# Performance work log

Measured on AMD Instinct MI355X. Metric: run time of the kernel, lower is better.

Reference implementation:

```python
import jax, jax.numpy as jnp
import numpy as np


def setup_inputs() -> dict:
    key = jax.random.key(0)
    k1, k2, k3, k4 = jax.random.split(key, 4)
    B, C, H, W = 4, 256, 64, 64
    Va = jax.random.normal(k1, (B, C, H, W), jnp.float32)
    Vb = jax.random.normal(k2, (B, C, H, W), jnp.float32)
    # nn.Linear(C, C, bias=False) weight, used as x @ W^T
    W_linear = jax.random.normal(k3, (C, C), jnp.float32) * 0.05
    # nn.Conv2d(C, 1, 1, bias=False) weight, init normal_(0, 0.01)
    W_gate = jax.random.normal(k4, (C,), jnp.float32) * 0.01
    return {"Va_output": Va, "Vb_output": Vb, "W_linear": W_linear,
            "W_gate": W_gate, "input_size": 512}


def reference(Va_output, Vb_output, W_linear, W_gate, input_size):
    B, C, H, W = Vb_output.shape
    A = H * W  # all_dim
    Va_flat = Va_output.reshape(B, C, A)  # [B, C, A]
    Vb_flat = Vb_output.reshape(B, C, A)
    # linear on transposed A-major tokens: Va_t @ W_linear^T -> [B, A, C]
    Va_corr = jnp.einsum('bca,dc->bad', Va_flat, W_linear)
    # correlation matrix S = Va_corr @ Vb_flat -> [B, A, A]
    S = jnp.einsum('bac,can->ban'[:3] + 'c,c' if False else 'bac,cn', Va_corr, Vb_flat) if False else jnp.einsum('bac,bcn->ban', Va_corr, Vb_flat)
    # S_c = softmax(S, dim=1); S_r = softmax(S^T, dim=1) = softmax(S, axis=2)^T
    S_c = jax.nn.softmax(S, axis=1)
    S_r = jnp.swapaxes(jax.nn.softmax(S, axis=2), 1, 2)
    Vb_att = jnp.einsum('bca,ban->bcn', Va_flat, S_r).reshape(B, C, H, W)
    Va_att = jnp.einsum('bca,ban->bcn', Vb_flat, S_c).reshape(B, C, H, W)
    # 1x1 gate conv (C -> 1, no bias) + sigmoid
    Va_mask = jax.nn.sigmoid(jnp.einsum('bchw,c->bhw', Va_att, W_gate))[:, None]
    Vb_mask = jax.nn.sigmoid(jnp.einsum('bchw,c->bhw', Vb_att, W_gate))[:, None]
    Va_out = jnp.concatenate([Va_att * Va_mask, Va_output], axis=1)  # [B, 2C, H, W]
    Vb_out = jnp.concatenate([Vb_att * Vb_mask, Vb_output], axis=1)
    return (Va_out, Vb_out, input_size)
```

## Files before the change

kernel.cpp:

```cpp
#include <hip/hip_runtime.h>

typedef _Float16 f16;
typedef f16 f16x8 __attribute__((ext_vector_type(8)));
typedef float f32x4 __attribute__((ext_vector_type(4)));
typedef short b16x8 __attribute__((ext_vector_type(8)));
typedef unsigned short u16;
typedef u16 u16x4 __attribute__((ext_vector_type(4)));

#define MFMA_F16(a,b,c)  __builtin_amdgcn_mfma_f32_16x16x32_f16((a),(b),(c),0,0,0)
#define MFMA_BF16(a,b,c) __builtin_amdgcn_mfma_f32_16x16x32_bf16((a),(b),(c),0,0,0)

static __device__ __forceinline__ u16 bf16rn(float f) {
    unsigned u = __builtin_bit_cast(unsigned, f);
    u += 0x7FFFu + ((u >> 16) & 1u);
    return (u16)(u >> 16);
}

typedef const __attribute__((address_space(1))) unsigned int* gas_p;
typedef __attribute__((address_space(3))) unsigned int* las_p;
static __device__ __forceinline__ void gll16(const void* g, void* l) {
    __builtin_amdgcn_global_load_lds((gas_p)g, (las_p)l, 16, 0, 0);
}

static constexpr int B_ = 4, C_ = 256, A_ = 4096;
static constexpr int CA   = C_ * A_;
static constexpr int BCA  = B_ * CA;
static constexpr int OUT_T = B_ * 2 * CA;
static constexpr size_t WS_Va16 = 0;
static constexpr size_t WS_Vb16 = WS_Va16 + (size_t)BCA;
static constexpr size_t WS_VaT  = WS_Vb16 + (size_t)BCA;
static constexpr size_t WS_VbT  = WS_VaT  + (size_t)BCA;
static constexpr size_t WS_Q1   = WS_VbT  + (size_t)BCA;
static constexpr size_t WS_W16  = WS_Q1   + (size_t)BCA;
static constexpr size_t WS_HALFS = WS_W16 + (size_t)(C_ * C_);

static constexpr float M0 = 48.0f;

__global__ void coatt_convw(const float* __restrict__ W, f16* __restrict__ W16) {
    int i = blockIdx.x * 256 + threadIdx.x;
    W16[i] = (f16)W[i];
}

__global__ void coatt_transpose(const float* __restrict__ Va,
                                const float* __restrict__ Vb,
                                u16* __restrict__ ws) {
    __shared__ f16 tile[64][72];
    int z = blockIdx.z; int b = z >> 1; int which = z & 1;
    const float* src = which ? Vb : Va;
    u16* cm = ws + (which ? WS_Vb16 : WS_Va16);
    f16* am = (f16*)(ws + (which ? WS_VbT : WS_VaT));
    int a0 = blockIdx.x * 64, c0 = blockIdx.y * 64;
    int t = threadIdx.x;
    int r = t >> 2, q = t & 3;

    const float* sp = src + (size_t)(b * C_ + c0 + r) * A_ + a0 + q * 16;
    f16 h[16] __attribute__((aligned(16)));
    u16 hb[16] __attribute__((aligned(16)));
#pragma unroll
    for (int i = 0; i < 4; ++i) {
        float4 v = *(const float4*)(sp + i * 4);
        h[i*4+0] = (f16)v.x; h[i*4+1] = (f16)v.y;
        h[i*4+2] = (f16)v.z; h[i*4+3] = (f16)v.w;
        hb[i*4+0] = bf16rn(v.x); hb[i*4+1] = bf16rn(v.y);
        hb[i*4+2] = bf16rn(v.z); hb[i*4+3] = bf16rn(v.w);
    }
    u16* cp = cm + (size_t)(b * C_ + c0 + r) * A_ + a0 + q * 16;
    *(u16x4*)(cp)      = *(const u16x4*)&hb[0];
    *(u16x4*)(cp + 4)  = *(const u16x4*)&hb[4];
    *(u16x4*)(cp + 8)  = *(const u16x4*)&hb[8];
    *(u16x4*)(cp + 12) = *(const u16x4*)&hb[12];
#pragma unroll
    for (int i = 0; i < 16; ++i) tile[r][q * 16 + i] = h[i];
    __syncthreads();
    f16 ht[16] __attribute__((aligned(16)));
#pragma unroll
    for (int i = 0; i < 16; ++i) ht[i] = tile[q * 16 + i][r];
    f16* ap = am + (size_t)(b * A_ + a0 + r) * C_ + c0 + q * 16;
    *(f16x8*)(ap)     = *(const f16x8*)&ht[0];
    *(f16x8*)(ap + 8) = *(const f16x8*)&ht[8];
}

__global__ __launch_bounds__(256) void coatt_q1(const f16* __restrict__ vat,
                                                const f16* __restrict__ w16,
                                                f16* __restrict__ q1) {
    int b = blockIdx.y; int a0 = blockIdx.x * 64;
    int tid = threadIdx.x, wave = tid >> 6, lane = tid & 63;
    int m = lane & 15, quad = lane >> 4;

    const f16* Ap = vat + (size_t)(b * A_ + a0 + wave * 16 + m) * C_ + quad * 8;
    f16x8 af[8];
#pragma unroll
    for (int kc = 0; kc < 8; ++kc) af[kc] = *(const f16x8*)(Ap + kc * 32);

    f32x4 acc[16];
#pragma unroll
    for (int t = 0; t < 16; ++t) acc[t] = (f32x4){0.f, 0.f, 0.f, 0.f};

#pragma unroll
    for (int kc = 0; kc < 8; ++kc) {
#pragma unroll
        for (int t = 0; t < 16; ++t) {
            f16x8 bf = *(const f16x8*)(w16 + (size_t)(t * 16 + m) * C_ + kc * 32 + quad * 8);
            acc[t] = MFMA_F16(af[kc], bf, acc[t]);
        }
    }
#pragma unroll
    for (int t = 0; t < 16; ++t) {
#pragma unroll
        for (int r = 0; r < 4; ++r) {
            int arow = a0 + wave * 16 + quad * 4 + r;
            q1[(size_t)(b * A_ + arow) * C_ + t * 16 + m] = (f16)acc[t][r];
        }
    }
}

__global__ __launch_bounds__(512, 2) void coatt_flash(const u16* __restrict__ ws,
                                                      const float* __restrict__ Wgate,
                                                      float* __restrict__ dout) {
    __shared__ __align__(16) char smem[151552];
    char* Plds = smem + 131072;
    float* Lsum = (float*)(smem + 149504);
    float* Gsum = (float*)(smem + 150528);
    float* Olds = (float*)smem;

    int p = blockIdx.x;
    int vc = p & 7;
    int b = vc & 3, att = vc >> 2;
    int n0 = (p >> 3) * 128;

    const f16 *Qp, *Kp; const u16* Vp; float* outp;
    if (att == 0) {
        Qp = (const f16*)(ws + WS_Q1)  + (size_t)b * CA;
        Kp = (const f16*)(ws + WS_VbT) + (size_t)b * CA;
        Vp = ws + WS_Va16 + (size_t)b * CA;
        outp = dout + (size_t)OUT_T + (size_t)b * 2 * CA;
    } else {
        Qp = (const f16*)(ws + WS_VbT) + (size_t)b * CA;
        Kp = (const f16*)(ws + WS_Q1)  + (size_t)b * CA;
        Vp = ws + WS_Vb16 + (size_t)b * CA;
        outp = dout + (size_t)b * 2 * CA;
    }

    int tid = threadIdx.x, wave = tid >> 6, lane = tid & 63;
    int i = wave >> 1, j = wave & 1;
    int m = lane & 15, quad = lane >> 4;

    f16x8 qf[2][8];
#pragma unroll
    for (int qt = 0; qt < 2; ++qt) {
        const f16* qr = Qp + (size_t)(n0 + i * 32 + qt * 16 + m) * C_ + quad * 8;
#pragma unroll
        for (int kc = 0; kc < 8; ++kc) qf[qt][kc] = *(const f16x8*)(qr + kc * 32);
    }

    f32x4 Oacc[2][8];
#pragma unroll
    for (int qt = 0; qt < 2; ++qt)
#pragma unroll
        for (int ct = 0; ct < 8; ++ct) Oacc[qt][ct] = (f32x4){0.f, 0.f, 0.f, 0.f};
    float lpart[2] = {0.f, 0.f};

    int kch = (lane & 31) ^ ((2 * wave + (lane >> 5)) & 7);
    int vch = (lane & 7) ^ ((lane >> 3) & 7);
    const f16* kgb = Kp + (size_t)(2 * wave + (lane >> 5)) * C_ + kch * 8;
    const u16* vgb = Vp + (size_t)(8 * wave + (lane >> 3)) * A_ + vch * 8;

    {
        const f16* kg = kgb;
        char* kl = smem + wave * 1024;
#pragma unroll
        for (int ii = 0; ii < 4; ++ii) gll16(kg + ii * 16 * C_, kl + ii * 8192);
        const u16* vg = vgb;
        char* vl = smem + 65536 + wave * 1024;
#pragma unroll
        for (int ii = 0; ii < 4; ++ii) gll16(vg + (size_t)ii * 64 * A_, vl + ii * 8192);
    }

    for (int kb = 0; kb < 64; ++kb) {
        int cur = kb & 1, nxt = cur ^ 1;
        char* Kc = smem + cur * 32768;
        char* Vc = smem + 65536 + cur * 32768;
        __syncthreads();

        if (kb < 63) {
            const f16* kg = kgb + (size_t)(kb + 1) * 64 * C_;
            char* kl = smem + nxt * 32768 + wave * 1024;
#pragma unroll
            for (int ii = 0; ii < 4; ++ii) gll16(kg + ii * 16 * C_, kl + ii * 8192);
        }

        f32x4 Sc[2][2];
#pragma unroll
        for (int kt = 0; kt < 2; ++kt)
#pragma unroll
            for (int qt = 0; qt < 2; ++qt) Sc[kt][qt] = (f32x4){0.f, 0.f, 0.f, 0.f};
#pragma unroll
        for (int kc = 0; kc < 8; ++kc) {
            f16x8 kf[2];
#pragma unroll
            for (int kt = 0; kt < 2; ++kt) {
                int kl_ = j * 32 + kt * 16 + m;
                kf[kt] = *(const f16x8*)(Kc + kl_ * 512 +
                                         (((kc * 4 + quad) ^ (kl_ & 7)) << 4));
            }
#pragma unroll
            for (int kt = 0; kt < 2; ++kt)
#pragma unroll
                for (int qt = 0; qt < 2; ++qt)
                    Sc[kt][qt] = MFMA_F16(kf[kt], qf[qt][kc], Sc[kt][qt]);
        }

#pragma unroll
        for (int qt = 0; qt < 2; ++qt) {
            int qg = i * 32 + qt * 16 + m;
#pragma unroll
            for (int kt = 0; kt < 2; ++kt) {
                u16x4 pk;
                float s4 = 0.f;
#pragma unroll
                for (int r = 0; r < 4; ++r) {
                    float pv = __expf(Sc[kt][qt][r] - M0);
                    s4 += pv;
                    pk[r] = bf16rn(pv);
                }
                lpart[qt] += s4;
                *(u16x4*)(Plds + qg * 144 + (j * 32 + kt * 16 + quad * 4) * 2) = pk;
            }
        }
        __syncthreads();

        if (kb < 63) {
            const u16* vg = vgb + (size_t)(kb + 1) * 64;
            char* vl = smem + 65536 + nxt * 32768 + wave * 1024;
#pragma unroll
            for (int ii = 0; ii < 4; ++ii) gll16(vg + (size_t)ii * 64 * A_, vl + ii * 8192);
        }

#pragma unroll
        for (int kt = 0; kt < 2; ++kt) {
            b16x8 pf[2];
#pragma unroll
            for (int qt = 0; qt < 2; ++qt) {
                int qg = i * 32 + qt * 16 + m;
                pf[qt] = *(const b16x8*)(Plds + qg * 144 + kt * 64 + quad * 16);
            }
#pragma unroll
            for (int ct = 0; ct < 8; ++ct) {
                int c = j * 128 + ct * 16 + m;
                b16x8 vf = *(const b16x8*)(Vc + c * 128 +
                                           (((kt * 4 + quad) ^ (c & 7)) << 4));
#pragma unroll
                for (int qt = 0; qt < 2; ++qt)
                    Oacc[qt][ct] = MFMA_BF16(pf[qt], vf, Oacc[qt][ct]);
            }
        }
    }

#pragma unroll
    for (int qt = 0; qt < 2; ++qt) {
        float v = lpart[qt];
        v += __shfl_xor(v, 16);
        v += __shfl_xor(v, 32);
        lpart[qt] = v;
    }
    __syncthreads();
    if (lane < 16) {
#pragma unroll
        for (int qt = 0; qt < 2; ++qt)
            Lsum[j * 128 + i * 32 + qt * 16 + lane] = lpart[qt];
    }
    __syncthreads();
    float inv[2][4];
#pragma unroll
    for (int qt = 0; qt < 2; ++qt)
#pragma unroll
        for (int r = 0; r < 4; ++r) {
            int q = i * 32 + qt * 16 + quad * 4 + r;
            inv[qt][r] = 1.0f / (Lsum[q] + Lsum[128 + q]);
        }
    float gp[2][4] = {{0.f,0.f,0.f,0.f},{0.f,0.f,0.f,0.f}};
#pragma unroll
    for (int ct = 0; ct < 8; ++ct) {
        float w = Wgate[j * 128 + ct * 16 + m];
#pragma unroll
        for (int qt = 0; qt < 2; ++qt)
#pragma unroll
            for (int r = 0; r < 4; ++r) {
                float o = Oacc[qt][ct][r] * inv[qt][r];
                Oacc[qt][ct][r] = o;
                gp[qt][r] += o * w;
            }
    }
#pragma unroll
    for (int qt = 0; qt < 2; ++qt)
#pragma unroll
        for (int r = 0; r < 4; ++r) {
            float v = gp[qt][r];
            v += __shfl_xor(v, 1); v += __shfl_xor(v, 2);
            v += __shfl_xor(v, 4); v += __shfl_xor(v, 8);
            gp[qt][r] = v;
        }
    if (m == 0) {
#pragma unroll
        for (int qt = 0; qt < 2; ++qt)
#pragma unroll
            for (int r = 0; r < 4; ++r)
                Gsum[j * 128 + i * 32 + qt * 16 + quad * 4 + r] = gp[qt][r];
    }
    __syncthreads();
#pragma unroll
    for (int qt = 0; qt < 2; ++qt)
#pragma unroll
        for (int r = 0; r < 4; ++r) {
            int q = i * 32 + qt * 16 + quad * 4 + r;
            float g = Gsum[q] + Gsum[128 + q];
            float msk = 1.0f / (1.0f + __expf(-g));
#pragma unroll
            for (int ct = 0; ct < 8; ++ct) Oacc[qt][ct][r] *= msk;
        }

    for (int hf = 0; hf < 2; ++hf) {
        __syncthreads();
        if (j == hf) {
#pragma unroll
            for (int ct = 0; ct < 8; ++ct)
#pragma unroll
                for (int qt = 0; qt < 2; ++qt)
#pragma unroll
                    for (int r = 0; r < 4; ++r)
                        Olds[(ct * 16 + m) * 132 + i * 32 + qt * 16 + quad * 4 + r] =
                            Oacc[qt][ct][r];
        }
        __syncthreads();
#pragma unroll
        for (int ii = 0; ii < 8; ++ii) {
            int ci = tid + ii * 512;
            int c = ci >> 5, ch = (ci & 31) * 4;
            float4 v = *(const float4*)(Olds + c * 132 + ch);
            *(float4*)(outp + (size_t)(hf * 128 + c) * A_ + n0 + ch) = v;
        }
    }
}

__global__ void coatt_copy(const float* __restrict__ Va, const float* __restrict__ Vb,
                           const int* __restrict__ psz, float* __restrict__ dout) {
    int base = blockIdx.x * 256 + threadIdx.x;
    const float4* va4 = (const float4*)Va;
    const float4* vb4 = (const float4*)Vb;
    float4* out4 = (float4*)dout;
#pragma unroll
    for (int i = 0; i < 4; ++i) {
        int idx = base + i * 524288;
        int t = idx >> 20;
        int r = idx & 1048575;
        int b = r >> 18;
        int rr = r & 262143;
        float4 v = t ? vb4[r] : va4[r];
        out4[(size_t)t * 2097152 + (size_t)b * 524288 + 262144 + rr] = v;
    }
    if (base == 0) dout[16777216] = (float)(*psz);
}

extern "C" void kernel_launch(void* const* d_in, const int* in_sizes, int n_in,
                              void* d_out, int out_size, void* d_ws, size_t ws_size,
                              hipStream_t stream) {
    const float* Va = (const float*)d_in[0];
    const float* Vb = (const float*)d_in[1];
    const float* Wl = (const float*)d_in[2];
    const float* Wg = (const float*)d_in[3];
    const int* psz  = (const int*)d_in[4];
    float* out = (float*)d_out;
    u16* ws = (u16*)d_ws;

    if (ws_size < WS_HALFS * sizeof(u16)) return;

    coatt_convw<<<256, 256, 0, stream>>>(Wl, (f16*)(ws + WS_W16));
    coatt_transpose<<<dim3(64, 4, 8), 256, 0, stream>>>(Va, Vb, ws);
    coatt_q1<<<dim3(64, 4), 256, 0, stream>>>((const f16*)(ws + WS_VaT),
                                              (const f16*)(ws + WS_W16),
                                              (f16*)(ws + WS_Q1));
    coatt_flash<<<256, 512, 0, stream>>>(ws, Wg, out);
    coatt_copy<<<2048, 256, 0, stream>>>(Va, Vb, psz, out);
}
```

Baseline: 271.0 us.

## Pre-tile Q/K/V into MFMA-friendly blocked layout and retile flash waves 2x4

The transpose and Q1 kernels now write the K/Q and V operands in a blocked 64-row tile layout, 16-byte chunks grouped by channel-chunk, so the flash kernel can fill LDS with contiguous per-lane global_load_lds copies and read fragments without XOR swizzling. The flash kernel's wave grid changes from 4x2 to 2x4: each wave now covers 64 queries by 16 keys for S and 64 queries by 64 channels for O, so each K fragment is reused across four query tiles. Partial softmax sums and gate sums are now reduced across four waves, and outputs go to LDS as float4 stores. This is meant to cut LDS address arithmetic, bank conflicts and strided global loads, at the cost of more query-fragment registers per wave and a possibly different LDS bank-conflict pattern.

```diff
diff --git a/kernel.cpp b/kernel.cpp
--- a/kernel.cpp
+++ b/kernel.cpp
@@ -44,11 +44,11 @@
 __global__ void coatt_transpose(const float* __restrict__ Va,
                                 const float* __restrict__ Vb,
                                 u16* __restrict__ ws) {
-    __shared__ f16 tile[64][72];
+    __shared__ f16 tile[64][73];
     int z = blockIdx.z; int b = z >> 1; int which = z & 1;
     const float* src = which ? Vb : Va;
-    u16* cm = ws + (which ? WS_Vb16 : WS_Va16);
-    f16* am = (f16*)(ws + (which ? WS_VbT : WS_VaT));
+    char* vt = (char*)(ws + (which ? WS_Vb16 : WS_Va16)) + (size_t)b * CA * 2;
+    char* kt = (char*)(ws + (which ? WS_VbT : WS_VaT)) + (size_t)b * CA * 2;
     int a0 = blockIdx.x * 64, c0 = blockIdx.y * 64;
     int t = threadIdx.x;
     int r = t >> 2, q = t & 3;
@@ -64,33 +64,35 @@
         hb[i*4+0] = bf16rn(v.x); hb[i*4+1] = bf16rn(v.y);
         hb[i*4+2] = bf16rn(v.z); hb[i*4+3] = bf16rn(v.w);
     }
-    u16* cp = cm + (size_t)(b * C_ + c0 + r) * A_ + a0 + q * 16;
-    *(u16x4*)(cp)      = *(const u16x4*)&hb[0];
-    *(u16x4*)(cp + 4)  = *(const u16x4*)&hb[4];
-    *(u16x4*)(cp + 8)  = *(const u16x4*)&hb[8];
-    *(u16x4*)(cp + 12) = *(const u16x4*)&hb[12];
+    char* vb8 = vt + (size_t)(a0 >> 6) * 32768 + (c0 + r) * 16;
+    *(u16x4*)(vb8 + (q * 2 + 0) * 4096 + 0) = *(const u16x4*)&hb[0];
+    *(u16x4*)(vb8 + (q * 2 + 0) * 4096 + 8) = *(const u16x4*)&hb[4];
+    *(u16x4*)(vb8 + (q * 2 + 1) * 4096 + 0) = *(const u16x4*)&hb[8];
+    *(u16x4*)(vb8 + (q * 2 + 1) * 4096 + 8) = *(const u16x4*)&hb[12];
 #pragma unroll
     for (int i = 0; i < 16; ++i) tile[r][q * 16 + i] = h[i];
     __syncthreads();
     f16 ht[16] __attribute__((aligned(16)));
 #pragma unroll
     for (int i = 0; i < 16; ++i) ht[i] = tile[q * 16 + i][r];
-    f16* ap = am + (size_t)(b * A_ + a0 + r) * C_ + c0 + q * 16;
-    *(f16x8*)(ap)     = *(const f16x8*)&ht[0];
-    *(f16x8*)(ap + 8) = *(const f16x8*)&ht[8];
-}
-
-__global__ __launch_bounds__(256) void coatt_q1(const f16* __restrict__ vat,
-                                                const f16* __restrict__ w16,
-                                                f16* __restrict__ q1) {
+    char* kb8 = kt + (size_t)(a0 >> 6) * 32768 + r * 16;
+    *(f16x8*)(kb8 + (size_t)(c0 / 8 + q * 2 + 0) * 1024) = *(const f16x8*)&ht[0];
+    *(f16x8*)(kb8 + (size_t)(c0 / 8 + q * 2 + 1) * 1024) = *(const f16x8*)&ht[8];
+}
+
+__global__ __launch_bounds__(256) void coatt_q1(const u16* __restrict__ ws_) {
+    const char* vat = (const char*)(ws_ + WS_VaT);
+    const f16* w16 = (const f16*)(ws_ + WS_W16);
+    char* q1 = (char*)(ws_ + WS_Q1);
     int b = blockIdx.y; int a0 = blockIdx.x * 64;
     int tid = threadIdx.x, wave = tid >> 6, lane = tid & 63;
     int m = lane & 15, quad = lane >> 4;
 
-    const f16* Ap = vat + (size_t)(b * A_ + a0 + wave * 16 + m) * C_ + quad * 8;
+    const char* Ab = vat + (size_t)b * CA * 2 + (size_t)(a0 >> 6) * 32768;
     f16x8 af[8];
 #pragma unroll
-    for (int kc = 0; kc < 8; ++kc) af[kc] = *(const f16x8*)(Ap + kc * 32);
+    for (int kc = 0; kc < 8; ++kc)
+        af[kc] = *(const f16x8*)(Ab + (kc * 4 + quad) * 1024 + (wave * 16 + m) * 16);
 
     f32x4 acc[16];
 #pragma unroll
@@ -104,12 +106,16 @@
             acc[t] = MFMA_F16(af[kc], bf, acc[t]);
         }
     }
+    char* Qb = q1 + (size_t)b * CA * 2 + (size_t)(a0 >> 6) * 32768;
 #pragma unroll
     for (int t = 0; t < 16; ++t) {
 #pragma unroll
         for (int r = 0; r < 4; ++r) {
-            int arow = a0 + wave * 16 + quad * 4 + r;
-            q1[(size_t)(b * A_ + arow) * C_ + t * 16 + m] = (f16)acc[t][r];
+            int al = wave * 16 + quad * 4 + r;
+            int d = t * 16 + m;
+            f16 v = (f16)acc[t][r];
+            *(u16*)(Qb + (size_t)(d >> 3) * 1024 + al * 16 + (d & 7) * 2) =
+                __builtin_bit_cast(u16, v);
         }
     }
 }
@@ -117,10 +123,10 @@
 __global__ __launch_bounds__(512, 2) void coatt_flash(const u16* __restrict__ ws,
                                                       const float* __restrict__ Wgate,
                                                       float* __restrict__ dout) {
-    __shared__ __align__(16) char smem[151552];
+    __shared__ __align__(16) char smem[153600];
     char* Plds = smem + 131072;
     float* Lsum = (float*)(smem + 149504);
-    float* Gsum = (float*)(smem + 150528);
+    float* Gsum = (float*)(smem + 151552);
     float* Olds = (float*)smem;
 
     int p = blockIdx.x;
@@ -128,52 +134,53 @@
     int b = vc & 3, att = vc >> 2;
     int n0 = (p >> 3) * 128;
 
-    const f16 *Qp, *Kp; const u16* Vp; float* outp;
+    const char *Qp, *Kp, *Vp; float* outp;
+    const char* base = (const char*)ws;
+    size_t boff = (size_t)b * CA * 2;
     if (att == 0) {
-        Qp = (const f16*)(ws + WS_Q1)  + (size_t)b * CA;
-        Kp = (const f16*)(ws + WS_VbT) + (size_t)b * CA;
-        Vp = ws + WS_Va16 + (size_t)b * CA;
+        Qp = base + WS_Q1 * 2 + boff;
+        Kp = base + WS_VbT * 2 + boff;
+        Vp = base + WS_Va16 * 2 + boff;
         outp = dout + (size_t)OUT_T + (size_t)b * 2 * CA;
     } else {
-        Qp = (const f16*)(ws + WS_VbT) + (size_t)b * CA;
-        Kp = (const f16*)(ws + WS_Q1)  + (size_t)b * CA;
-        Vp = ws + WS_Vb16 + (size_t)b * CA;
+        Qp = base + WS_VbT * 2 + boff;
+        Kp = base + WS_Q1 * 2 + boff;
+        Vp = base + WS_Vb16 * 2 + boff;
         outp = dout + (size_t)b * 2 * CA;
     }
 
     int tid = threadIdx.x, wave = tid >> 6, lane = tid & 63;
-    int i = wave >> 1, j = wave & 1;
+    int iq = wave >> 2, jq = wave & 3;
     int m = lane & 15, quad = lane >> 4;
 
-    f16x8 qf[2][8];
-#pragma unroll
-    for (int qt = 0; qt < 2; ++qt) {
-        const f16* qr = Qp + (size_t)(n0 + i * 32 + qt * 16 + m) * C_ + quad * 8;
-#pragma unroll
-        for (int kc = 0; kc < 8; ++kc) qf[qt][kc] = *(const f16x8*)(qr + kc * 32);
-    }
-
-    f32x4 Oacc[2][8];
-#pragma unroll
-    for (int qt = 0; qt < 2; ++qt)
-#pragma unroll
-        for (int ct = 0; ct < 8; ++ct) Oacc[qt][ct] = (f32x4){0.f, 0.f, 0.f, 0.f};
-    float lpart[2] = {0.f, 0.f};
-
-    int kch = (lane & 31) ^ ((2 * wave + (lane >> 5)) & 7);
-    int vch = (lane & 7) ^ ((lane >> 3) & 7);
-    const f16* kgb = Kp + (size_t)(2 * wave + (lane >> 5)) * C_ + kch * 8;
-    const u16* vgb = Vp + (size_t)(8 * wave + (lane >> 3)) * A_ + vch * 8;
-
+    f16x8 qf[4][8];
     {
-        const f16* kg = kgb;
-        char* kl = smem + wave * 1024;
-#pragma unroll
-        for (int ii = 0; ii < 4; ++ii) gll16(kg + ii * 16 * C_, kl + ii * 8192);
-        const u16* vg = vgb;
-        char* vl = smem + 65536 + wave * 1024;
-#pragma unroll
-        for (int ii = 0; ii < 4; ++ii) gll16(vg + (size_t)ii * 64 * A_, vl + ii * 8192);
+        const char* qb = Qp + (size_t)((n0 >> 6) + iq) * 32768;
+#pragma unroll
+        for (int qt = 0; qt < 4; ++qt)
+#pragma unroll
+            for (int kc = 0; kc < 8; ++kc)
+                qf[qt][kc] = *(const f16x8*)(qb + (kc * 4 + quad) * 1024 +
+                                             (qt * 16 + m) * 16);
+    }
+
+    f32x4 Oacc[4][4];
+#pragma unroll
+    for (int qt = 0; qt < 4; ++qt)
+#pragma unroll
+        for (int ct = 0; ct < 4; ++ct) Oacc[qt][ct] = (f32x4){0.f, 0.f, 0.f, 0.f};
+    float lpart[4] = {0.f, 0.f, 0.f, 0.f};
+
+    const char* ksrc = Kp + wave * 1024 + lane * 16;
+    const char* vsrc = Vp + wave * 1024 + lane * 16;
+
+    {
+#pragma unroll
+        for (int ii = 0; ii < 4; ++ii)
+            gll16(ksrc + ii * 8192, smem + wave * 1024 + ii * 8192);
+#pragma unroll
+        for (int ii = 0; ii < 4; ++ii)
+            gll16(vsrc + ii * 8192, smem + 65536 + wave * 1024 + ii * 8192);
     }
 
     for (int kb = 0; kb < 64; ++kb) {
@@ -183,81 +190,68 @@
         __syncthreads();
 
         if (kb < 63) {
-            const f16* kg = kgb + (size_t)(kb + 1) * 64 * C_;
+            const char* kg = ksrc + (size_t)(kb + 1) * 32768;
             char* kl = smem + nxt * 32768 + wave * 1024;
 #pragma unroll
-            for (int ii = 0; ii < 4; ++ii) gll16(kg + ii * 16 * C_, kl + ii * 8192);
-        }
-
-        f32x4 Sc[2][2];
-#pragma unroll
-        for (int kt = 0; kt < 2; ++kt)
-#pragma unroll
-            for (int qt = 0; qt < 2; ++qt) Sc[kt][qt] = (f32x4){0.f, 0.f, 0.f, 0.f};
+            for (int ii = 0; ii < 4; ++ii) gll16(kg + ii * 8192, kl + ii * 8192);
+        }
+
+        f32x4 Sc[4];
+#pragma unroll
+        for (int qt = 0; qt < 4; ++qt) Sc[qt] = (f32x4){0.f, 0.f, 0.f, 0.f};
 #pragma unroll
         for (int kc = 0; kc < 8; ++kc) {
-            f16x8 kf[2];
-#pragma unroll
-            for (int kt = 0; kt < 2; ++kt) {
-                int kl_ = j * 32 + kt * 16 + m;
-                kf[kt] = *(const f16x8*)(Kc + kl_ * 512 +
-                                         (((kc * 4 + quad) ^ (kl_ & 7)) << 4));
+            f16x8 kf = *(const f16x8*)(Kc + (kc * 4 + quad) * 1024 +
+                                       (jq * 16 + m) * 16);
+#pragma unroll
+            for (int qt = 0; qt < 4; ++qt)
+                Sc[qt] = MFMA_F16(kf, qf[qt][kc], Sc[qt]);
+        }
+
+#pragma unroll
+        for (int qt = 0; qt < 4; ++qt) {
+            int q = iq * 64 + qt * 16 + m;
+            u16x4 pk;
+            float s4 = 0.f;
+#pragma unroll
+            for (int r = 0; r < 4; ++r) {
+                float pv = __expf(Sc[qt][r] - M0);
+                s4 += pv;
+                pk[r] = bf16rn(pv);
             }
-#pragma unroll
-            for (int kt = 0; kt < 2; ++kt)
-#pragma unroll
-                for (int qt = 0; qt < 2; ++qt)
-                    Sc[kt][qt] = MFMA_F16(kf[kt], qf[qt][kc], Sc[kt][qt]);
-        }
-
-#pragma unroll
-        for (int qt = 0; qt < 2; ++qt) {
-            int qg = i * 32 + qt * 16 + m;
-#pragma unroll
-            for (int kt = 0; kt < 2; ++kt) {
-                u16x4 pk;
-                float s4 = 0.f;
-#pragma unroll
-                for (int r = 0; r < 4; ++r) {
-                    float pv = __expf(Sc[kt][qt][r] - M0);
-                    s4 += pv;
-                    pk[r] = bf16rn(pv);
-                }
-                lpart[qt] += s4;
-                *(u16x4*)(Plds + qg * 144 + (j * 32 + kt * 16 + quad * 4) * 2) = pk;
+            lpart[qt] += s4;
+            *(u16x4*)(Plds + q * 144 + jq * 32 + quad * 8) = pk;
+        }
+        __syncthreads();
+
+        if (kb < 63) {
+            const char* vg = vsrc + (size_t)(kb + 1) * 32768;
+            char* vl = smem + 65536 + nxt * 32768 + wave * 1024;
+#pragma unroll
+            for (int ii = 0; ii < 4; ++ii) gll16(vg + ii * 8192, vl + ii * 8192);
+        }
+
+#pragma unroll
+        for (int s = 0; s < 2; ++s) {
+            b16x8 pf[4];
+#pragma unroll
+            for (int qt = 0; qt < 4; ++qt) {
+                int q = iq * 64 + qt * 16 + m;
+                pf[qt] = *(const b16x8*)(Plds + q * 144 + s * 64 + quad * 16);
             }
-        }
-        __syncthreads();
-
-        if (kb < 63) {
-            const u16* vg = vgb + (size_t)(kb + 1) * 64;
-            char* vl = smem + 65536 + nxt * 32768 + wave * 1024;
-#pragma unroll
-            for (int ii = 0; ii < 4; ++ii) gll16(vg + (size_t)ii * 64 * A_, vl + ii * 8192);
-        }
-
-#pragma unroll
-        for (int kt = 0; kt < 2; ++kt) {
-            b16x8 pf[2];
-#pragma unroll
-            for (int qt = 0; qt < 2; ++qt) {
-                int qg = i * 32 + qt * 16 + m;
-                pf[qt] = *(const b16x8*)(Plds + qg * 144 + kt * 64 + quad * 16);
-            }
-#pragma unroll
-            for (int ct = 0; ct < 8; ++ct) {
-                int c = j * 128 + ct * 16 + m;
-                b16x8 vf = *(const b16x8*)(Vc + c * 128 +
-                                           (((kt * 4 + quad) ^ (c & 7)) << 4));
-#pragma unroll
-                for (int qt = 0; qt < 2; ++qt)
+#pragma unroll
+            for (int ct = 0; ct < 4; ++ct) {
+                int c = jq * 64 + ct * 16 + m;
+                b16x8 vf = *(const b16x8*)(Vc + (s * 4 + quad) * 4096 + c * 16);
+#pragma unroll
+                for (int qt = 0; qt < 4; ++qt)
                     Oacc[qt][ct] = MFMA_BF16(pf[qt], vf, Oacc[qt][ct]);
             }
         }
     }
 
 #pragma unroll
-    for (int qt = 0; qt < 2; ++qt) {
+    for (int qt = 0; qt < 4; ++qt) {
         float v = lpart[qt];
         v += __shfl_xor(v, 16);
         v += __shfl_xor(v, 32);
@@ -266,24 +260,26 @@
     __syncthreads();
     if (lane < 16) {
 #pragma unroll
-        for (int qt = 0; qt < 2; ++qt)
-            Lsum[j * 128 + i * 32 + qt * 16 + lane] = lpart[qt];
+        for (int qt = 0; qt < 4; ++qt)
+            Lsum[wave * 64 + qt * 16 + lane] = lpart[qt];
     }
     __syncthreads();
-    float inv[2][4];
-#pragma unroll
-    for (int qt = 0; qt < 2; ++qt)
+    float inv[4][4];
+#pragma unroll
+    for (int qt = 0; qt < 4; ++qt)
 #pragma unroll
         for (int r = 0; r < 4; ++r) {
-            int q = i * 32 + qt * 16 + quad * 4 + r;
-            inv[qt][r] = 1.0f / (Lsum[q] + Lsum[128 + q]);
-        }
-    float gp[2][4] = {{0.f,0.f,0.f,0.f},{0.f,0.f,0.f,0.f}};
-#pragma unroll
-    for (int ct = 0; ct < 8; ++ct) {
-        float w = Wgate[j * 128 + ct * 16 + m];
-#pragma unroll
-        for (int qt = 0; qt < 2; ++qt)
+            int ql = qt * 16 + quad * 4 + r;
+            float s = Lsum[(iq * 4 + 0) * 64 + ql] + Lsum[(iq * 4 + 1) * 64 + ql] +
+                      Lsum[(iq * 4 + 2) * 64 + ql] + Lsum[(iq * 4 + 3) * 64 + ql];
+            inv[qt][r] = 1.0f / s;
+        }
+    float gp[4][4] = {{0,0,0,0},{0,0,0,0},{0,0,0,0},{0,0,0,0}};
+#pragma unroll
+    for (int ct = 0; ct < 4; ++ct) {
+        float w = Wgate[jq * 64 + ct * 16 + m];
+#pragma unroll
+        for (int qt = 0; qt < 4; ++qt)
 #pragma unroll
             for (int r = 0; r < 4; ++r) {
                 float o = Oacc[qt][ct][r] * inv[qt][r];
@@ -292,7 +288,7 @@
             }
     }
 #pragma unroll
-    for (int qt = 0; qt < 2; ++qt)
+    for (int qt = 0; qt < 4; ++qt)
 #pragma unroll
         for (int r = 0; r < 4; ++r) {
             float v = gp[qt][r];
@@ -302,34 +298,37 @@
         }
     if (m == 0) {
 #pragma unroll
-        for (int qt = 0; qt < 2; ++qt)
+        for (int qt = 0; qt < 4; ++qt)
 #pragma unroll
             for (int r = 0; r < 4; ++r)
-                Gsum[j * 128 + i * 32 + qt * 16 + quad * 4 + r] = gp[qt][r];
+                Gsum[wave * 64 + qt * 16 + quad * 4 + r] = gp[qt][r];
     }
     __syncthreads();
 #pragma unroll
-    for (int qt = 0; qt < 2; ++qt)
+    for (int qt = 0; qt < 4; ++qt)
 #pragma unroll
         for (int r = 0; r < 4; ++r) {
-            int q = i * 32 + qt * 16 + quad * 4 + r;
-            float g = Gsum[q] + Gsum[128 + q];
+            int ql = qt * 16 + quad * 4 + r;
+            float g = Gsum[(iq * 4 + 0) * 64 + ql] + Gsum[(iq * 4 + 1) * 64 + ql] +
+                      Gsum[(iq * 4 + 2) * 64 + ql] + Gsum[(iq * 4 + 3) * 64 + ql];
             float msk = 1.0f / (1.0f + __expf(-g));
 #pragma unroll
-            for (int ct = 0; ct < 8; ++ct) Oacc[qt][ct][r] *= msk;
+            for (int ct = 0; ct < 4; ++ct) Oacc[qt][ct][r] *= msk;
         }
 
     for (int hf = 0; hf < 2; ++hf) {
         __syncthreads();
-        if (j == hf) {
-#pragma unroll
-            for (int ct = 0; ct < 8; ++ct)
-#pragma unroll
-                for (int qt = 0; qt < 2; ++qt)
-#pragma unroll
-                    for (int r = 0; r < 4; ++r)
-                        Olds[(ct * 16 + m) * 132 + i * 32 + qt * 16 + quad * 4 + r] =
-                            Oacc[qt][ct][r];
+        if ((jq >> 1) == hf) {
+#pragma unroll
+            for (int ct = 0; ct < 4; ++ct)
+#pragma unroll
+                for (int qt = 0; qt < 4; ++qt) {
+                    int cl = (jq & 1) * 64 + ct * 16 + m;
+                    float4 v;
+                    v.x = Oacc[qt][ct][0]; v.y = Oacc[qt][ct][1];
+                    v.z = Oacc[qt][ct][2]; v.w = Oacc[qt][ct][3];
+                    *(float4*)(Olds + cl * 132 + iq * 64 + qt * 16 + quad * 4) = v;
+                }
         }
         __syncthreads();
 #pragma unroll
@@ -376,9 +375,7 @@
 
     coatt_convw<<<256, 256, 0, stream>>>(Wl, (f16*)(ws + WS_W16));
     coatt_transpose<<<dim3(64, 4, 8), 256, 0, stream>>>(Va, Vb, ws);
-    coatt_q1<<<dim3(64, 4), 256, 0, stream>>>((const f16*)(ws + WS_VaT),
-                                              (const f16*)(ws + WS_W16),
-                                              (f16*)(ws + WS_Q1));
+    coatt_q1<<<dim3(64, 4), 256, 0, stream>>>(ws);
     coatt_flash<<<256, 512, 0, stream>>>(ws, Wg, out);
     coatt_copy<<<2048, 256, 0, stream>>>(Va, Vb, psz, out);
 }
```

New measurement: 268.1 us. Within noise of the previous version (-1.1%).
